# Kernel tuning notes

Hardware: AMD Instinct MI355X
Metric: run time of the kernel (lower is better)

## Reference

```python
import jax, jax.numpy as jnp
import numpy as np

B, S, D = 4, 2048, 768
H, R = 12, 8
Dh = D // H


def setup_inputs() -> dict:
    key = jax.random.key(0)
    ks = jax.random.split(key, 12)
    s_in = 1.0 / np.sqrt(D)
    s_r = 1.0 / np.sqrt(R)
    return {
        "x": jax.random.normal(ks[0], (B, S, D), jnp.float32),
        "Wq0": jax.random.normal(ks[1], (D, D), jnp.float32) * s_in,
        "Aq": jax.random.normal(ks[2], (D, R), jnp.float32) * s_in,
        "Bq": jax.random.normal(ks[3], (R, D), jnp.float32) * s_r,
        "Wk0": jax.random.normal(ks[4], (D, D), jnp.float32) * s_in,
        "Ak": jax.random.normal(ks[5], (D, R), jnp.float32) * s_in,
        "Bk": jax.random.normal(ks[6], (R, D), jnp.float32) * s_r,
        "Wv0": jax.random.normal(ks[7], (D, D), jnp.float32) * s_in,
        "Av": jax.random.normal(ks[8], (D, R), jnp.float32) * s_in,
        "Bv": jax.random.normal(ks[9], (R, D), jnp.float32) * s_r,
        "Wo": jax.random.normal(ks[10], (D, D), jnp.float32) * s_in,
        "bo": jnp.zeros((D,), jnp.float32),
    }


def _lora(x, W0, A, Bm):
    # x @ W0 + (x @ A) @ B  -- low-rank adapter on frozen W0
    return x @ W0 + (x @ A) @ Bm


def _split_heads(t):
    # [B,S,D] -> [B,H,S,Dh]
    return t.reshape(B, S, H, Dh).transpose(0, 2, 1, 3)


def reference(x, Wq0, Aq, Bq, Wk0, Ak, Bk, Wv0, Av, Bv, Wo, bo):
    q = _split_heads(_lora(x, Wq0, Aq, Bq))
    k = _split_heads(_lora(x, Wk0, Ak, Bk))
    v = _split_heads(_lora(x, Wv0, Av, Bv))
    scale = 1.0 / jnp.sqrt(jnp.asarray(Dh, x.dtype))
    scores = jnp.einsum("bhqd,bhkd->bhqk", q, k) * scale  # [B,H,S,S]
    weights = jax.nn.softmax(scores, axis=-1)
    attn = jnp.einsum("bhqk,bhkd->bhqd", weights, v)
    concat = attn.transpose(0, 2, 1, 3).reshape(B, S, D)
    return concat @ Wo + bo
```

## Files before the change

### kernel.cpp

```cpp
#include <hip/hip_runtime.h>
#include <hip/hip_bf16.h>


typedef unsigned short ushort_t;
typedef __bf16 bf16x8 __attribute__((ext_vector_type(8)));
typedef float f32x4 __attribute__((ext_vector_type(4)));
typedef float f32x16 __attribute__((ext_vector_type(16)));
typedef unsigned short ushort8 __attribute__((ext_vector_type(8)));
typedef unsigned short ushort4_t __attribute__((ext_vector_type(4)));
typedef unsigned int uint4v __attribute__((ext_vector_type(4)));
typedef __attribute__((address_space(1))) unsigned int gu32;
typedef __attribute__((address_space(3))) unsigned int lu32;

__device__ __forceinline__ unsigned short f2bf(float f) {
  unsigned int u = __builtin_bit_cast(unsigned int, f);
  u += 0x7fffu + ((u >> 16) & 1u);
  return (unsigned short)(u >> 16);
}

__device__ __forceinline__ void gld_lds16(const void* g, void* s) {
  __builtin_amdgcn_global_load_lds((gu32*)(unsigned long long)g,
                                   (lu32*)(unsigned int)(unsigned long long)s,
                                   16, 0, 0);
}

__device__ __forceinline__ f32x4 mfma16(bf16x8 a, bf16x8 b, f32x4 c) {
  return __builtin_amdgcn_mfma_f32_16x16x32_bf16(a, b, c, 0, 0, 0);
}

__device__ __forceinline__ f32x16 mfma32(bf16x8 a, bf16x8 b, f32x16 c) {
  return __builtin_amdgcn_mfma_f32_32x32x16_bf16(a, b, c, 0, 0, 0);
}

__device__ __forceinline__ unsigned int cvtpk(float a, float b) {
  unsigned int r;
  asm("v_cvt_pk_bf16_f32 %0, %1, %2" : "=v"(r) : "v"(a), "v"(b));
  return r;
}

__global__ __launch_bounds__(256) void prep_weights(
    const float* __restrict__ Wq0, const float* __restrict__ Aq, const float* __restrict__ Bq,
    const float* __restrict__ Wk0, const float* __restrict__ Ak, const float* __restrict__ Bk,
    const float* __restrict__ Wv0, const float* __restrict__ Av, const float* __restrict__ Bv,
    const float* __restrict__ Wo,
    ushort_t* __restrict__ WeffT, ushort_t* __restrict__ WoT)
{
  __shared__ float tile[32][33];
  __shared__ float tA[32][8];
  __shared__ float tB[8][32];
  const int mat = blockIdx.y;
  const int kt = blockIdx.x / 24, nt = blockIdx.x % 24;
  const int k0 = kt * 32, n0 = nt * 32;
  const float* W0 = (mat == 0) ? Wq0 : (mat == 1) ? Wk0 : (mat == 2) ? Wv0 : Wo;
  const float* Am = (mat == 0) ? Aq : (mat == 1) ? Ak : (mat == 2) ? Av : nullptr;
  const float* Bm = (mat == 0) ? Bq : (mat == 1) ? Bk : (mat == 2) ? Bv : nullptr;
  const int tid = threadIdx.x;
#pragma unroll
  for (int i = 0; i < 4; i++) {
    int rr = i * 8 + (tid >> 5), c = tid & 31;
    tile[rr][c] = W0[(k0 + rr) * 768 + n0 + c];
  }
  if (Am) {
    tA[tid >> 3][tid & 7] = Am[(k0 + (tid >> 3)) * 8 + (tid & 7)];
    tB[tid >> 5][tid & 31] = Bm[(tid >> 5) * 768 + n0 + (tid & 31)];
  }
  __syncthreads();
#pragma unroll
  for (int i = 0; i < 4; i++) {
    int kk = tid & 31;
    int nn = i * 8 + (tid >> 5);
    float val = tile[kk][nn];
    if (Am) {
#pragma unroll
      for (int rr = 0; rr < 8; rr++) val += tA[kk][rr] * tB[rr][nn];
    }
    int n = n0 + nn, kg = k0 + kk;
    if (mat < 3) WeffT[((long)mat * 768 + n) * 768 + kg] = f2bf(val);
    else         WoT[(long)n * 768 + kg] = f2bf(val);
  }
}

__global__ __launch_bounds__(256) void cast_x(const float* __restrict__ x,
                                              ushort_t* __restrict__ xb)
{
  long i = (long)blockIdx.x * 256 + threadIdx.x;
  const float4* xp = (const float4*)x;
  float4 a = xp[i * 2], c = xp[i * 2 + 1];
  ushort8 rv;
  rv[0] = f2bf(a.x); rv[1] = f2bf(a.y); rv[2] = f2bf(a.z); rv[3] = f2bf(a.w);
  rv[4] = f2bf(c.x); rv[5] = f2bf(c.y); rv[6] = f2bf(c.z); rv[7] = f2bf(c.w);
  *(ushort8*)&xb[i * 8] = rv;
}

template <int MODE>
__global__ __launch_bounds__(256) void gemm_bt(
    const ushort_t* __restrict__ A, const ushort_t* __restrict__ Bt,
    ushort_t* __restrict__ q, ushort_t* __restrict__ kbuf, ushort_t* __restrict__ vt,
    float* __restrict__ out, const float* __restrict__ bo)
{
  constexpr int K = 768;
  __shared__ __align__(16) ushort_t As[128 * 64];
  __shared__ __align__(16) ushort_t Bs[128 * 64];
  const int tid = threadIdx.x;
  const int l = tid & 63, w = tid >> 6;
  const int wm = w >> 1, wn = w & 1;
  const int lr = l & 15, lg = l >> 4;
  const long rowBase = (long)blockIdx.x * 128;
  const long colBase = (long)blockIdx.y * 128;
  f32x4 acc[4][4] = {};

  for (int k0 = 0; k0 < K; k0 += 64) {
    __syncthreads();
#pragma unroll
    for (int i = 0; i < 4; i++) {
      int ci = i * 256 + tid;
      gld_lds16(A + (rowBase + (ci >> 3)) * K + k0 + (ci & 7) * 8, &As[ci * 8]);
    }
#pragma unroll
    for (int i = 0; i < 4; i++) {
      int ci = i * 256 + tid;
      gld_lds16(Bt + (colBase + (ci >> 3)) * K + k0 + (ci & 7) * 8, &Bs[ci * 8]);
    }
    asm volatile("s_waitcnt vmcnt(0)" ::: "memory");
    __syncthreads();
#pragma unroll
    for (int ks = 0; ks < 2; ks++) {
      bf16x8 af[4], bf[4];
#pragma unroll
      for (int m = 0; m < 4; m++)
        af[m] = *(const bf16x8*)&As[(wm * 64 + m * 16 + lr) * 64 + ks * 32 + lg * 8];
#pragma unroll
      for (int n = 0; n < 4; n++)
        bf[n] = *(const bf16x8*)&Bs[(wn * 64 + n * 16 + lr) * 64 + ks * 32 + lg * 8];
#pragma unroll
      for (int m = 0; m < 4; m++)
#pragma unroll
        for (int n = 0; n < 4; n++)
          acc[m][n] = mfma16(af[m], bf[n], acc[m][n]);
    }
  }

  if (MODE == 0) {
    const int mat = (int)(colBase / 768);
    __syncthreads();
    ushort_t* myscr = (w < 2) ? &As[w * 4096] : &Bs[(w - 2) * 4096];
    if (mat == 2) {
      const long cb = colBase - 1536;
#pragma unroll
      for (int m = 0; m < 4; m++) {
        int sp0 = m * 16 + ((lg & 1) << 3) + ((lg >> 1) << 2);
#pragma unroll
        for (int n = 0; n < 4; n++) {
          int lcol = n * 16 + lr;
          int ch = (sp0 >> 3) ^ (lcol & 7);
          ushort4_t pk;
#pragma unroll
          for (int r = 0; r < 4; r++) pk[r] = f2bf(acc[m][n][r]);
          *(ushort4_t*)&myscr[lcol * 64 + ch * 8 + (sp0 & 7)] = pk;
        }
      }
      asm volatile("s_waitcnt lgkmcnt(0)" ::: "memory");
      const long sB = rowBase + wm * 64;
      const long bI = sB >> 11, sL = sB & 2047;
      const long cg = cb + wn * 64;
#pragma unroll
      for (int it = 0; it < 8; it++) {
        int cl = (l >> 3) + it * 8;
        int ch = (l & 7) ^ (cl & 7);
        ushort8 vv = *(const ushort8*)&myscr[cl * 64 + ch * 8];
        *(ushort8*)&vt[(bI * 768 + cg + cl) * 2048 + sL + (l & 7) * 8] = vv;
      }
    } else {
      ushort_t* dst = (mat == 0) ? q : kbuf;
      const float scl = (mat == 0) ? 0.125f * 1.4426950408889634f : 1.0f;
      const long cb = colBase - (long)mat * 768;
#pragma unroll
      for (int m = 0; m < 4; m++)
#pragma unroll
        for (int n = 0; n < 4; n++)
#pragma unroll
          for (int r = 0; r < 4; r++) {
            int lrow = m * 16 + lg * 4 + r, lcol = n * 16 + lr;
            int ch = (lcol >> 3) ^ (lrow & 7);
            myscr[lrow * 64 + ch * 8 + (lcol & 7)] = f2bf(acc[m][n][r] * scl);
          }
      asm volatile("s_waitcnt lgkmcnt(0)" ::: "memory");
      const long cg = cb + wn * 64;
#pragma unroll
      for (int it = 0; it < 8; it++) {
        int rl = (l >> 3) + it * 8;
        int ch = (l & 7) ^ (rl & 7);
        ushort8 vv = *(const ushort8*)&myscr[rl * 64 + ch * 8];
        *(ushort8*)&dst[(rowBase + wm * 64 + rl) * 768 + cg + (l & 7) * 8] = vv;
      }
    }
  } else {
#pragma unroll
    for (int m = 0; m < 4; m++)
#pragma unroll
      for (int n = 0; n < 4; n++) {
        long col = colBase + wn * 64 + n * 16 + lr;
        float bv = bo[col];
#pragma unroll
        for (int r = 0; r < 4; r++) {
          long row = rowBase + wm * 64 + m * 16 + lg * 4 + r;
          out[row * 768 + col] = acc[m][n][r] + bv;
        }
      }
  }
}

__global__ __launch_bounds__(256) void attn_fwd(
    const ushort_t* __restrict__ Q, const ushort_t* __restrict__ Kg,
    const ushort_t* __restrict__ VtG, ushort_t* __restrict__ O)
{
  constexpr int D = 768, S = 2048;
  __shared__ __align__(16) ushort_t Ks[3][64 * 64];
  __shared__ __align__(16) ushort_t Vs[3][64 * 64];
  __shared__ float Lrow[4][32];
  const int tid = threadIdx.x;
  const int l = tid & 63, w = tid >> 6;
  const int q32 = l & 31, hi = l >> 5;
  const int i = blockIdx.x;
  const int xcd = i & 7, j = i >> 3;
  const int bh = xcd * 6 + (j >> 4);
  const int q0 = (j & 15) * 128;
  const int b = bh / 12, h = bh % 12;
  const ushort_t* Qb = Q + (long)b * S * D + h * 64;
  const ushort_t* Kb = Kg + (long)b * S * D + h * 64;
  const ushort_t* Vb = VtG + ((long)b * 768 + h * 64) * S;

  bf16x8 qf[4];
  {
    const ushort_t* qrow = Qb + (long)(q0 + w * 32 + q32) * D + hi * 8;
#pragma unroll
    for (int ks = 0; ks < 4; ks++) qf[ks] = *(const bf16x8*)&qrow[ks * 16];
  }

  int koff[2], voff[2];
#pragma unroll
  for (int it = 0; it < 2; it++) {
    int ci = it * 256 + tid, r = ci >> 3, c = ci & 7;
    koff[it] = r * D + ((c ^ (r & 7)) * 8);
    voff[it] = r * S + ((c ^ (r & 7)) * 8);
  }
  const int swz = q32 & 7;
  int rdoff[4];
#pragma unroll
  for (int ks = 0; ks < 4; ks++) rdoff[ks] = ((ks * 2 + hi) ^ swz) * 8;

  f32x16 oA = {}, oB = {};
  float psum = 0.f;

  auto STAGE = [&](int kt, int bi) {
    const ushort_t* kp = Kb + (long)kt * 64 * D;
    const ushort_t* vp = Vb + kt * 64;
#pragma unroll
    for (int it = 0; it < 2; it++)
      gld_lds16(kp + koff[it], &Ks[bi][(it * 256 + tid) * 8]);
#pragma unroll
    for (int it = 0; it < 2; it++)
      gld_lds16(vp + voff[it], &Vs[bi][(it * 256 + tid) * 8]);
  };

  STAGE(0, 0);
  int cur = 0;

  for (int kt = 0; kt < 32; kt++) {
    int nxt = cur + 1; if (nxt == 3) nxt = 0;
    STAGE((kt + 1) & 31, nxt);
    asm volatile("s_waitcnt vmcnt(4)" ::: "memory");
    __builtin_amdgcn_s_barrier();

    const ushort_t* ksb = &Ks[cur][0];
    const ushort_t* vsb = &Vs[cur][0];

    f32x16 s0 = {}, s1 = {};
    __builtin_amdgcn_s_setprio(1);
#pragma unroll
    for (int ks = 0; ks < 4; ks++) {
      bf16x8 kf0 = *(const bf16x8*)&ksb[q32 * 64 + rdoff[ks]];
      bf16x8 kf1 = *(const bf16x8*)&ksb[(32 + q32) * 64 + rdoff[ks]];
      s0 = mfma32(kf0, qf[ks], s0);
      s1 = mfma32(kf1, qf[ks], s1);
    }
    __builtin_amdgcn_s_setprio(0);

    unsigned int pw[16];
#pragma unroll
    for (int u = 0; u < 8; u++) {
      float a0 = __builtin_amdgcn_exp2f(s0[2 * u]);
      float a1 = __builtin_amdgcn_exp2f(s0[2 * u + 1]);
      psum += a0 + a1;
      pw[u] = cvtpk(a0, a1);
    }
#pragma unroll
    for (int u = 0; u < 8; u++) {
      float a0 = __builtin_amdgcn_exp2f(s1[2 * u]);
      float a1 = __builtin_amdgcn_exp2f(s1[2 * u + 1]);
      psum += a0 + a1;
      pw[8 + u] = cvtpk(a0, a1);
    }

    __builtin_amdgcn_s_setprio(1);
#pragma unroll
    for (int ks = 0; ks < 4; ks++) {
      uint4v w4 = {pw[4 * ks], pw[4 * ks + 1], pw[4 * ks + 2], pw[4 * ks + 3]};
      bf16x8 pa = __builtin_bit_cast(bf16x8, w4);
      bf16x8 vf0 = *(const bf16x8*)&vsb[q32 * 64 + rdoff[ks]];
      bf16x8 vf1 = *(const bf16x8*)&vsb[(32 + q32) * 64 + rdoff[ks]];
      oA = mfma32(pa, vf0, oA);
      oB = mfma32(pa, vf1, oB);
    }
    __builtin_amdgcn_s_setprio(0);

    cur = nxt;
  }

  float tot = psum + __shfl_xor(psum, 32, 64);
  Lrow[w][q32] = tot;
  asm volatile("s_waitcnt lgkmcnt(0)" ::: "memory");

#pragma unroll
  for (int reg = 0; reg < 16; reg++) {
    int row = (reg & 3) + 8 * (reg >> 2) + 4 * hi;
    float inv = 1.0f / Lrow[w][row];
    long base = ((long)b * S + q0 + w * 32 + row) * D + h * 64 + q32;
    O[base] = f2bf(oA[reg] * inv);
    O[base + 32] = f2bf(oB[reg] * inv);
  }
}

extern "C" void kernel_launch(void* const* d_in, const int* in_sizes, int n_in,
                              void* d_out, int out_size, void* d_ws, size_t ws_size,
                              hipStream_t stream)
{
  const float* x   = (const float*)d_in[0];
  const float* Wq0 = (const float*)d_in[1];
  const float* Aq  = (const float*)d_in[2];
  const float* Bq  = (const float*)d_in[3];
  const float* Wk0 = (const float*)d_in[4];
  const float* Ak  = (const float*)d_in[5];
  const float* Bk  = (const float*)d_in[6];
  const float* Wv0 = (const float*)d_in[7];
  const float* Av  = (const float*)d_in[8];
  const float* Bv  = (const float*)d_in[9];
  const float* Wo  = (const float*)d_in[10];
  const float* bo  = (const float*)d_in[11];
  float* out = (float*)d_out;

  char* ws = (char*)d_ws;
  const long SZ = 8192L * 768 * 2;
  ushort_t* xb    = (ushort_t*)(ws);
  ushort_t* Qb    = (ushort_t*)(ws + SZ);
  ushort_t* Kb    = (ushort_t*)(ws + 2 * SZ);
  ushort_t* Vt    = (ushort_t*)(ws + 3 * SZ);
  ushort_t* At    = (ushort_t*)(ws + 4 * SZ);
  ushort_t* WeffT = (ushort_t*)(ws + 5 * SZ);
  ushort_t* WoT   = (ushort_t*)(ws + 5 * SZ + 2304L * 768 * 2);

  hipLaunchKernelGGL(prep_weights, dim3(576, 4), dim3(256), 0, stream,
                     Wq0, Aq, Bq, Wk0, Ak, Bk, Wv0, Av, Bv, Wo, WeffT, WoT);
  hipLaunchKernelGGL(cast_x, dim3(3072), dim3(256), 0, stream, x, xb);
  hipLaunchKernelGGL((gemm_bt<0>), dim3(64, 18), dim3(256), 0, stream,
                     xb, WeffT, Qb, Kb, Vt, (float*)nullptr, (const float*)nullptr);
  hipLaunchKernelGGL(attn_fwd, dim3(768), dim3(256), 0, stream, Qb, Kb, Vt, At);
  hipLaunchKernelGGL((gemm_bt<1>), dim3(64, 6), dim3(256), 0, stream,
                     At, WoT, (ushort_t*)nullptr, (ushort_t*)nullptr, (ushort_t*)nullptr,
                     out, bo);
}
```

Baseline: 177.0 us.

## Double-buffer GEMM K loop with swizzled LDS; compute attention row sums via MFMA

```diff
diff --git a/kernel.cpp b/kernel.cpp
--- a/kernel.cpp
+++ b/kernel.cpp
@@ -99,8 +99,9 @@
     float* __restrict__ out, const float* __restrict__ bo)
 {
   constexpr int K = 768;
-  __shared__ __align__(16) ushort_t As[128 * 64];
-  __shared__ __align__(16) ushort_t Bs[128 * 64];
+  constexpr int NT = K / 64;
+  __shared__ __align__(16) ushort_t As[2][128 * 64];
+  __shared__ __align__(16) ushort_t Bs[2][128 * 64];
   const int tid = threadIdx.x;
   const int l = tid & 63, w = tid >> 6;
   const int wm = w >> 1, wn = w & 1;
@@ -109,41 +110,64 @@
   const long colBase = (long)blockIdx.y * 128;
   f32x4 acc[4][4] = {};
 
-  for (int k0 = 0; k0 < K; k0 += 64) {
-    __syncthreads();
-#pragma unroll
-    for (int i = 0; i < 4; i++) {
-      int ci = i * 256 + tid;
-      gld_lds16(A + (rowBase + (ci >> 3)) * K + k0 + (ci & 7) * 8, &As[ci * 8]);
-    }
-#pragma unroll
-    for (int i = 0; i < 4; i++) {
-      int ci = i * 256 + tid;
-      gld_lds16(Bt + (colBase + (ci >> 3)) * K + k0 + (ci & 7) * 8, &Bs[ci * 8]);
-    }
-    asm volatile("s_waitcnt vmcnt(0)" ::: "memory");
-    __syncthreads();
+  int soff[4];
+#pragma unroll
+  for (int i = 0; i < 4; i++) {
+    int ci = i * 256 + tid, r = ci >> 3, c = ci & 7;
+    soff[i] = r * K + ((c ^ (r & 7)) * 8);
+  }
+  int rdoff[2];
+#pragma unroll
+  for (int ks = 0; ks < 2; ks++) rdoff[ks] = ((ks * 4 + lg) ^ (lr & 7)) * 8;
+
+  const ushort_t* Abase = A + rowBase * K;
+  const ushort_t* Bbase = Bt + colBase * K;
+
+  auto STAGE = [&](int t, int bi) {
+    const ushort_t* ap = Abase + t * 64;
+    const ushort_t* bp = Bbase + t * 64;
+#pragma unroll
+    for (int i = 0; i < 4; i++)
+      gld_lds16(ap + soff[i], &As[bi][(i * 256 + tid) * 8]);
+#pragma unroll
+    for (int i = 0; i < 4; i++)
+      gld_lds16(bp + soff[i], &Bs[bi][(i * 256 + tid) * 8]);
+  };
+
+  STAGE(0, 0);
+
+  for (int t = 0; t < NT; t++) {
+    const int cur = t & 1;
+    if (t + 1 < NT) {
+      STAGE(t + 1, cur ^ 1);
+      asm volatile("s_waitcnt vmcnt(8)" ::: "memory");
+    } else {
+      asm volatile("s_waitcnt vmcnt(0)" ::: "memory");
+    }
+    __builtin_amdgcn_s_barrier();
 #pragma unroll
     for (int ks = 0; ks < 2; ks++) {
       bf16x8 af[4], bf[4];
 #pragma unroll
       for (int m = 0; m < 4; m++)
-        af[m] = *(const bf16x8*)&As[(wm * 64 + m * 16 + lr) * 64 + ks * 32 + lg * 8];
+        af[m] = *(const bf16x8*)&As[cur][(wm * 64 + m * 16 + lr) * 64 + rdoff[ks]];
 #pragma unroll
       for (int n = 0; n < 4; n++)
-        bf[n] = *(const bf16x8*)&Bs[(wn * 64 + n * 16 + lr) * 64 + ks * 32 + lg * 8];
+        bf[n] = *(const bf16x8*)&Bs[cur][(wn * 64 + n * 16 + lr) * 64 + rdoff[ks]];
 #pragma unroll
       for (int m = 0; m < 4; m++)
 #pragma unroll
         for (int n = 0; n < 4; n++)
           acc[m][n] = mfma16(af[m], bf[n], acc[m][n]);
     }
+    asm volatile("" ::: "memory");
+    __builtin_amdgcn_s_barrier();
   }
 
   if (MODE == 0) {
     const int mat = (int)(colBase / 768);
     __syncthreads();
-    ushort_t* myscr = (w < 2) ? &As[w * 4096] : &Bs[(w - 2) * 4096];
+    ushort_t* myscr = (w < 2) ? &As[0][w * 4096] : &Bs[0][(w - 2) * 4096];
     if (mat == 2) {
       const long cb = colBase - 1536;
 #pragma unroll
@@ -215,9 +239,8 @@
     const ushort_t* __restrict__ VtG, ushort_t* __restrict__ O)
 {
   constexpr int D = 768, S = 2048;
-  __shared__ __align__(16) ushort_t Ks[3][64 * 64];
-  __shared__ __align__(16) ushort_t Vs[3][64 * 64];
-  __shared__ float Lrow[4][32];
+  __shared__ __align__(16) ushort_t Ks[2][64 * 64];
+  __shared__ __align__(16) ushort_t Vs[2][64 * 64];
   const int tid = threadIdx.x;
   const int l = tid & 63, w = tid >> 6;
   const int q32 = l & 31, hi = l >> 5;
@@ -249,8 +272,11 @@
 #pragma unroll
   for (int ks = 0; ks < 4; ks++) rdoff[ks] = ((ks * 2 + hi) ^ swz) * 8;
 
-  f32x16 oA = {}, oB = {};
-  float psum = 0.f;
+  bf16x8 ones;
+#pragma unroll
+  for (int e = 0; e < 8; e++) ones[e] = (__bf16)1.0f;
+
+  f32x16 oA = {}, oB = {}, osum = {};
 
   auto STAGE = [&](int kt, int bi) {
     const ushort_t* kp = Kb + (long)kt * 64 * D;
@@ -264,11 +290,10 @@
   };
 
   STAGE(0, 0);
-  int cur = 0;
 
   for (int kt = 0; kt < 32; kt++) {
-    int nxt = cur + 1; if (nxt == 3) nxt = 0;
-    STAGE((kt + 1) & 31, nxt);
+    const int cur = kt & 1;
+    STAGE((kt + 1) & 31, cur ^ 1);
     asm volatile("s_waitcnt vmcnt(4)" ::: "memory");
     __builtin_amdgcn_s_barrier();
 
@@ -291,14 +316,12 @@
     for (int u = 0; u < 8; u++) {
       float a0 = __builtin_amdgcn_exp2f(s0[2 * u]);
       float a1 = __builtin_amdgcn_exp2f(s0[2 * u + 1]);
-      psum += a0 + a1;
       pw[u] = cvtpk(a0, a1);
     }
 #pragma unroll
     for (int u = 0; u < 8; u++) {
       float a0 = __builtin_amdgcn_exp2f(s1[2 * u]);
       float a1 = __builtin_amdgcn_exp2f(s1[2 * u + 1]);
-      psum += a0 + a1;
       pw[8 + u] = cvtpk(a0, a1);
     }
 
@@ -311,20 +334,18 @@
       bf16x8 vf1 = *(const bf16x8*)&vsb[(32 + q32) * 64 + rdoff[ks]];
       oA = mfma32(pa, vf0, oA);
       oB = mfma32(pa, vf1, oB);
+      osum = mfma32(pa, ones, osum);
     }
     __builtin_amdgcn_s_setprio(0);
 
-    cur = nxt;
-  }
-
-  float tot = psum + __shfl_xor(psum, 32, 64);
-  Lrow[w][q32] = tot;
-  asm volatile("s_waitcnt lgkmcnt(0)" ::: "memory");
+    asm volatile("" ::: "memory");
+    __builtin_amdgcn_s_barrier();
+  }
 
 #pragma unroll
   for (int reg = 0; reg < 16; reg++) {
     int row = (reg & 3) + 8 * (reg >> 2) + 4 * hi;
-    float inv = 1.0f / Lrow[w][row];
+    float inv = 1.0f / osum[reg];
     long base = ((long)b * S + q0 + w * 32 + row) * D + h * 64 + q32;
     O[base] = f2bf(oA[reg] * inv);
     O[base + 32] = f2bf(oB[reg] * inv);
```

New measurement: 153.1 us. 13.5% less time.
